# Performance work log

Hardware: AMD Instinct MI355X
Metric: run time of the kernel (lower is better)

The kernel has to match this reference:

```python
import jax, jax.numpy as jnp
import numpy as np

B, H, W, CIN, COUT, KH, KW = 16, 64, 64, 256, 256, 3, 3


def setup_inputs() -> dict:
    key = jax.random.key(0)
    k1, k2, k3 = jax.random.split(key, 3)
    x = jax.random.normal(k1, (B, H, W, CIN), dtype=jnp.float32)
    style = jax.random.normal(k2, (B, CIN), dtype=jnp.float32)
    # glorot-ish scale for the base kernel
    kernel = jax.random.normal(k3, (KH, KW, CIN, COUT), dtype=jnp.float32) * 0.05
    return {"x": x, "style": style, "kernel": kernel}


def reference(x, style, kernel):
    b = x.shape[0]
    cout = kernel.shape[-1]
    # Modulate: per-sample weights [B, kh, kw, Cin, Cout]
    w = kernel[None] * (style[:, None, None, :, None] + 1.0)
    # Demodulate: L2 normalize over (kh, kw, Cin) per (sample, out-channel)
    w = w / jnp.sqrt(jnp.sum(jnp.square(w), axis=(1, 2, 3), keepdims=True) + 1e-8)
    # Batch-as-groups grouped conv: x -> [1, B*Cin, H, W]
    xg = jnp.transpose(x, (0, 3, 1, 2)).reshape(1, -1, x.shape[1], x.shape[2])
    # w -> [kh, kw, Cin, B*Cout]
    wg = jnp.transpose(w, (1, 2, 3, 0, 4)).reshape(w.shape[1], w.shape[2], w.shape[3], -1)
    y = jax.lax.conv_general_dilated(
        xg, wg,
        window_strides=(1, 1),
        padding='SAME',
        dimension_numbers=('NCHW', 'HWIO', 'NCHW'),
        feature_group_count=b,
    )
    # [1, B*Cout, H, W] -> [B, H, W, Cout]
    y = y.reshape(b, cout, y.shape[2], y.shape[3])
    return jnp.transpose(y, (0, 2, 3, 1))
```

## Files before the change

### kernel.cpp

```cpp
#include <hip/hip_runtime.h>


#define HH 64
#define WW 64
#define CI 256
#define CO 256
#define XP 66
#define CIPITCH 40
#define XCOLS 66

typedef float    f32x4 __attribute__((ext_vector_type(4)));
typedef _Float16 f16x8 __attribute__((ext_vector_type(8)));
typedef __fp16   fp16x2 __attribute__((ext_vector_type(2)));

__device__ __forceinline__ unsigned pk2(float a, float b) {
    fp16x2 h = __builtin_amdgcn_cvt_pkrtz(a, b);
    return __builtin_bit_cast(unsigned, h);
}

__global__ __launch_bounds__(256) void prep(
    const float* __restrict__ kern,
    const float* __restrict__ style,
    ushort* __restrict__ Wt2,
    float* __restrict__ scale2)
{
    __shared__ ushort tile[64][65];
    __shared__ float  sqt[64][65];
    __shared__ float  st2l[16][64];

    const int kt = blockIdx.x >> 2;
    const int ct = blockIdx.x & 3;
    const int k0 = kt * 64, c0 = ct * 64;
    const int ci0 = k0 & 255;
    const int tid = threadIdx.x;
    const int r = tid >> 2, q = tid & 3;

    #pragma unroll
    for (int p = 0; p < 4; ++p) {
        const int i = p * 256 + tid;
        const int bb = i >> 6, rr = i & 63;
        const float s = style[bb * CI + ci0 + rr] + 1.0f;
        st2l[bb][rr] = s * s;
    }

    const float* src = kern + (size_t)(k0 + r) * CO + c0 + q * 16;
    #pragma unroll
    for (int j = 0; j < 16; ++j) {
        const float v = src[j];
        _Float16 h = (_Float16)v;
        tile[q * 16 + j][r] = __builtin_bit_cast(unsigned short, h);
        sqt[r][q * 16 + j] = v * v;
    }
    __syncthreads();

    const int co_w = c0 + r;
    #pragma unroll
    for (int j = 0; j < 16; ++j) {
        const int k   = k0 + q * 16 + j;
        const int t9  = k >> 8;
        const int rem = k & 255;
        const int cc  = rem >> 5;
        const int fq  = (rem >> 3) & 3;
        const int e   = k & 7;
        Wt2[((((size_t)cc * 9 + t9) * 4 + fq) * 256 + co_w) * 8 + e] =
            tile[r][q * 16 + j];
    }

    const int co = tid & 63;
    const int bq = tid >> 6;
    float acc[4] = {0.f, 0.f, 0.f, 0.f};
    #pragma unroll 4
    for (int rr = 0; rr < 64; ++rr) {
        const float s = sqt[rr][co];
        #pragma unroll
        for (int bb = 0; bb < 4; ++bb)
            acc[bb] += s * st2l[bq * 4 + bb][rr];
    }
    #pragma unroll
    for (int bb = 0; bb < 4; ++bb)
        atomicAdd(&scale2[(bq * 4 + bb) * CO + c0 + co], acc[bb]);
}

__global__ __launch_bounds__(256) void xmod_k(
    const float* __restrict__ x,
    const float* __restrict__ style,
    ushort* __restrict__ Xm)
{
    const int b  = blockIdx.x / XP;
    const int hh = blockIdx.x - b * XP;
    const int tid = threadIdx.x;
    ushort* dst = Xm + ((size_t)(b * XP + hh)) * XP * CI;

    if (hh == 0 || hh == XP - 1) {
        const uint4 z = {0, 0, 0, 0};
        #pragma unroll
        for (int p = 0; p < 9; ++p) {
            const int t = p * 256 + tid;
            if (t < 2112) *(uint4*)(dst + t * 8) = z;
        }
        return;
    }

    const int l = tid & 63;
    const int q = tid >> 6;
    const int ci0 = l * 4;
    const int rg = hh - 1;

    f32x4 st = *(const f32x4*)(style + b * CI + ci0);
    st.x += 1.f; st.y += 1.f; st.z += 1.f; st.w += 1.f;

    const float* srow = x + ((size_t)(b * HH + rg)) * WW * CI + ci0;
    #pragma unroll
    for (int k = 0; k < 17; ++k) {
        const int cc = q + 4 * k;
        if (cc < XP) {
            uint2 u = {0, 0};
            if (cc >= 1 && cc <= WW) {
                const f32x4 v = *(const f32x4*)(srow + (size_t)(cc - 1) * CI);
                const f32x4 m = v * st;
                u.x = pk2(m.x, m.y);
                u.y = pk2(m.z, m.w);
            }
            *(uint2*)(dst + cc * CI + ci0) = u;
        }
    }
}

__global__ __launch_bounds__(256, 3) void gemm_dma(
    const ushort* __restrict__ Xm,
    const ushort* __restrict__ Wt2,
    const float* __restrict__ scale2,
    float* __restrict__ y)
{
    __shared__ __align__(16) ushort xs[10240];
    __shared__ __align__(16) ushort bs[3 * 4096];

    const int tid  = threadIdx.x;
    const int lane = tid & 63;
    const int wave = tid >> 6;

    const int mtile = blockIdx.x >> 1;
    const int n0    = (blockIdx.x & 1) * 128;
    const int p0    = mtile * 128;
    const int b     = p0 >> 12;
    const int h0    = (p0 >> 6) & 63;

    const int wm = (wave & 1) * 64;
    const int wn = (wave >> 1) * 64;
    const int fr = lane & 15;
    const int fq = lane >> 4;

    const ushort* xb = Xm + (size_t)b * XP * XP * CI;

    auto issue_xs = [&](int cn) {
        #pragma unroll
        for (int p = 0; p < 5; ++p) {
            const int task = p * 256 + tid;
            const int rc = task >> 2;
            const int ch = (task & 3) ^ ((rc >> 1) & 3);
            const int off = (rc < 264)
                ? (((h0 + rc / 66) * XP + (rc % 66)) * CI + ch * 8 + cn * 32)
                : 0;
            const ushort* g = xb + off;
            const ushort* l = xs + (p * 256 + (tid & ~63)) * 8;
            __builtin_amdgcn_global_load_lds(
                (const __attribute__((address_space(1))) void*)g,
                (__attribute__((address_space(3))) void*)l,
                16, 0, 0);
        }
    };

    auto issue_tile = [&](int cn, int t9n, int bufn) {
        const ushort* gb = Wt2 + ((size_t)((cn * 9 + t9n) * 4) * 256 + n0) * 8;
        #pragma unroll
        for (int p = 0; p < 2; ++p) {
            const int task = p * 256 + tid;
            const ushort* g = gb + (size_t)(((task >> 7) << 8) + (task & 127)) * 8;
            const ushort* l = bs + bufn * 4096 + (p * 256 + (tid & ~63)) * 8;
            __builtin_amdgcn_global_load_lds(
                (const __attribute__((address_space(1))) void*)g,
                (__attribute__((address_space(3))) void*)l,
                16, 0, 0);
        }
    };

    f32x4 acc[4][4] = {};

    issue_xs(0);
    issue_tile(0, 0, 0);
    issue_tile(0, 1, 1);

    for (int c = 0; c < 8; ++c) {
        #pragma unroll
        for (int t9 = 0; t9 < 9; ++t9) {
            if (c == 7 && t9 == 8)
                asm volatile("s_waitcnt vmcnt(0) lgkmcnt(0)" ::: "memory");
            else
                asm volatile("s_waitcnt vmcnt(2) lgkmcnt(0)" ::: "memory");
            __builtin_amdgcn_s_barrier();

            const int dh  = t9 / 3;
            const int dw  = t9 - dh * 3;
            const int buf = t9 % 3;

            if (t9 < 8) {
                const int t2 = (t9 + 2 >= 9) ? t9 - 7 : t9 + 2;
                const int c2 = (t9 >= 7) ? c + 1 : c;
                if (c2 < 8) issue_tile(c2, t2, t2 % 3);

                f16x8 af[4], bf[4];
                #pragma unroll
                for (int i = 0; i < 4; ++i) {
                    const int mb = wm + i * 16;
                    const int rc = ((mb >> 6) + dh) * XCOLS + (mb & 63) + fr + dw;
                    af[i] = *(const f16x8*)(xs + rc * 32 + ((fq ^ ((rc >> 1) & 3)) * 8));
                }
                #pragma unroll
                for (int j = 0; j < 4; ++j)
                    bf[j] = *(const f16x8*)(bs + buf * 4096 + fq * 1024
                                            + (wn + j * 16 + fr) * 8);
                __builtin_amdgcn_s_setprio(1);
                #pragma unroll
                for (int i = 0; i < 4; ++i)
                    #pragma unroll
                    for (int j = 0; j < 4; ++j)
                        acc[i][j] = __builtin_amdgcn_mfma_f32_16x16x32_f16(
                            af[i], bf[j], acc[i][j], 0, 0, 0);
                __builtin_amdgcn_s_setprio(0);
            } else {
                f16x8 af[4], bf[4];
                #pragma unroll
                for (int i = 0; i < 4; ++i) {
                    const int mb = wm + i * 16;
                    const int rc = ((mb >> 6) + dh) * XCOLS + (mb & 63) + fr + dw;
                    af[i] = *(const f16x8*)(xs + rc * 32 + ((fq ^ ((rc >> 1) & 3)) * 8));
                }
                #pragma unroll
                for (int j = 0; j < 4; ++j)
                    bf[j] = *(const f16x8*)(bs + buf * 4096 + fq * 1024
                                            + (wn + j * 16 + fr) * 8);
                if (c < 7) {
                    asm volatile("s_waitcnt lgkmcnt(0)" ::: "memory");
                    __builtin_amdgcn_s_barrier();
                    issue_xs(c + 1);
                    issue_tile(c + 1, 1, 1);
                }
                __builtin_amdgcn_s_setprio(1);
                #pragma unroll
                for (int i = 0; i < 4; ++i)
                    #pragma unroll
                    for (int j = 0; j < 4; ++j)
                        acc[i][j] = __builtin_amdgcn_mfma_f32_16x16x32_f16(
                            af[i], bf[j], acc[i][j], 0, 0, 0);
                __builtin_amdgcn_s_setprio(0);
            }
        }
    }

    float sc[4];
    #pragma unroll
    for (int j = 0; j < 4; ++j)
        sc[j] = __frsqrt_rn(scale2[b * CO + n0 + wn + j * 16 + fr] + 1e-8f);
    #pragma unroll
    for (int i = 0; i < 4; ++i) {
        const int m_base = p0 + wm + i * 16 + fq * 4;
        #pragma unroll
        for (int j = 0; j < 4; ++j) {
            float* yp = y + (size_t)m_base * CO + n0 + wn + j * 16 + fr;
            #pragma unroll
            for (int r = 0; r < 4; ++r)
                yp[(size_t)r * CO] = acc[i][j][r] * sc[j];
        }
    }
}

__global__ __launch_bounds__(256) void gemm_lds(
    const float* __restrict__ x,
    const ushort* __restrict__ Wt2,
    const float* __restrict__ style,
    const float* __restrict__ scale2,
    float* __restrict__ y)
{
    __shared__ __align__(16) ushort xsf[4 * XCOLS * CIPITCH];
    __shared__ __align__(16) ushort bs[3 * 4096];
    __shared__ float s_style[CI];

    const int tid  = threadIdx.x;
    const int lane = tid & 63;
    const int wave = tid >> 6;

    const int mtile = blockIdx.x >> 1;
    const int n0    = (blockIdx.x & 1) * 128;
    const int p0    = mtile * 128;
    const int b     = p0 >> 12;
    const int h0    = (p0 >> 6) & 63;

    s_style[tid] = style[b * CI + tid] + 1.0f;

    const int wm = (wave & 1) * 64;
    const int wn = (wave >> 1) * 64;
    const int fr = lane & 15;
    const int fq = lane >> 4;
    const int xlane = fr * CIPITCH + fq * 8;

    auto issue_tile = [&](int cn, int t9n, int bufn) {
        const ushort* gb = Wt2 + ((size_t)((cn * 9 + t9n) * 4) * 256 + n0) * 8;
        #pragma unroll
        for (int p = 0; p < 2; ++p) {
            const int task = p * 256 + tid;
            const ushort* g = gb + (size_t)(((task >> 7) << 8) + (task & 127)) * 8;
            const ushort* l = bs + bufn * 4096 + (p * 256 + (tid & ~63)) * 8;
            __builtin_amdgcn_global_load_lds(
                (const __attribute__((address_space(1))) void*)g,
                (__attribute__((address_space(3))) void*)l,
                16, 0, 0);
        }
    };

    f32x4 acc[4][4] = {};

    issue_tile(0, 0, 0);
    issue_tile(0, 1, 1);

    for (int c = 0; c < 8; ++c) {
        #pragma unroll
        for (int t9 = 0; t9 < 9; ++t9) {
            asm volatile("s_waitcnt vmcnt(2) lgkmcnt(0)" ::: "memory");
            __builtin_amdgcn_s_barrier();

            if (t9 == 0) {
                #pragma unroll
                for (int p = 0; p < 9; ++p) {
                    const int task = p * 256 + tid;
                    if (task < 2112) {
                        const int rowcol = task >> 3;
                        const int chunk  = task & 7;
                        const int row = rowcol / XCOLS;
                        const int col = rowcol - row * XCOLS;
                        const int rg = h0 - 1 + row;
                        const int cg = col - 1;
                        f32x4 v = {0.f, 0.f, 0.f, 0.f};
                        if ((unsigned)rg < 64u && (unsigned)cg < 64u)
                            v = *(const f32x4*)(x + ((size_t)((b * HH + rg) * WW + cg)) * CI
                                                  + c * 32 + chunk * 4);
                        const f32x4 st = *(const f32x4*)(s_style + c * 32 + chunk * 4);
                        const f32x4 m = v * st;
                        uint2 u;
                        u.x = pk2(m.x, m.y);
                        u.y = pk2(m.z, m.w);
                        *(uint2*)(xsf + rowcol * CIPITCH + chunk * 4) = u;
                    }
                }
                asm volatile("s_waitcnt lgkmcnt(0)" ::: "memory");
                __builtin_amdgcn_s_barrier();
            }

            {
                const int t2 = (t9 + 2 >= 9) ? t9 - 7 : t9 + 2;
                const int c2 = (t9 >= 7) ? c + 1 : c;
                if (c2 < 8) issue_tile(c2, t2, t2 % 3);
            }

            const int buf = t9 % 3;
            const int dh  = t9 / 3;
            const int dw  = t9 - dh * 3;

            f16x8 af[4], bf[4];
            #pragma unroll
            for (int i = 0; i < 4; ++i) {
                const int mb   = wm + i * 16;
                const int mrow = (mb >> 6) + dh;
                const int mcol = (mb & 63) + dw;
                af[i] = *(const f16x8*)(xsf + (mrow * XCOLS + mcol) * CIPITCH + xlane);
            }
            #pragma unroll
            for (int j = 0; j < 4; ++j)
                bf[j] = *(const f16x8*)(bs + buf * 4096 + fq * 1024
                                        + (wn + j * 16 + fr) * 8);
            #pragma unroll
            for (int i = 0; i < 4; ++i)
                #pragma unroll
                for (int j = 0; j < 4; ++j)
                    acc[i][j] = __builtin_amdgcn_mfma_f32_16x16x32_f16(
                        af[i], bf[j], acc[i][j], 0, 0, 0);
        }
    }

    float sc[4];
    #pragma unroll
    for (int j = 0; j < 4; ++j)
        sc[j] = __frsqrt_rn(scale2[b * CO + n0 + wn + j * 16 + fr] + 1e-8f);
    #pragma unroll
    for (int i = 0; i < 4; ++i) {
        const int m_base = p0 + wm + i * 16 + fq * 4;
        #pragma unroll
        for (int j = 0; j < 4; ++j) {
            float* yp = y + (size_t)m_base * CO + n0 + wn + j * 16 + fr;
            #pragma unroll
            for (int r = 0; r < 4; ++r)
                yp[(size_t)r * CO] = acc[i][j][r] * sc[j];
        }
    }
}

extern "C" void kernel_launch(void* const* d_in, const int* in_sizes, int n_in,
                              void* d_out, int out_size, void* d_ws, size_t ws_size,
                              hipStream_t stream) {
    const float* x     = (const float*)d_in[0];
    const float* style = (const float*)d_in[1];
    const float* kern  = (const float*)d_in[2];
    float* out = (float*)d_out;

    float*  scale2 = (float*)d_ws;
    ushort* Wt2    = (ushort*)((char*)d_ws + 16384);

    const size_t xm_off  = 16384 + 1179648;
    const size_t xm_size = (size_t)16 * XP * XP * CI * 2;

    hipMemsetAsync(scale2, 0, 16 * CO * sizeof(float), stream);
    prep<<<144, 256, 0, stream>>>(kern, style, Wt2, scale2);

    if (ws_size >= xm_off + xm_size) {
        ushort* Xm = (ushort*)((char*)d_ws + xm_off);
        xmod_k<<<16 * XP, 256, 0, stream>>>(x, style, Xm);
        gemm_dma<<<512 * 2, 256, 0, stream>>>(Xm, Wt2, scale2, out);
    } else {
        gemm_lds<<<512 * 2, 256, 0, stream>>>(x, Wt2, style, scale2, out);
    }
}
```

Measured before the change: 209.0 us.

## Give each wave private double-buffered weight tiles to drop per-step block barriers

```diff
diff --git a/kernel.cpp b/kernel.cpp
--- a/kernel.cpp
+++ b/kernel.cpp
@@ -126,14 +126,14 @@
     }
 }
 
-__global__ __launch_bounds__(256, 3) void gemm_dma(
+__global__ __launch_bounds__(256) void gemm_dma(
     const ushort* __restrict__ Xm,
     const ushort* __restrict__ Wt2,
     const float* __restrict__ scale2,
     float* __restrict__ y)
 {
     __shared__ __align__(16) ushort xs[10240];
-    __shared__ __align__(16) ushort bs[3 * 4096];
+    __shared__ __align__(16) ushort bsw[4][2][2048];
 
     const int tid  = threadIdx.x;
     const int lane = tid & 63;
@@ -170,13 +170,13 @@
         }
     };
 
-    auto issue_tile = [&](int cn, int t9n, int bufn) {
-        const ushort* gb = Wt2 + ((size_t)((cn * 9 + t9n) * 4) * 256 + n0) * 8;
-        #pragma unroll
-        for (int p = 0; p < 2; ++p) {
-            const int task = p * 256 + tid;
-            const ushort* g = gb + (size_t)(((task >> 7) << 8) + (task & 127)) * 8;
-            const ushort* l = bs + bufn * 4096 + (p * 256 + (tid & ~63)) * 8;
+    auto issue_bs = [&](int T, int bufn) {
+        const ushort* gb = Wt2 + (size_t)T * 8192 + (size_t)(n0 + wn) * 8
+                           + (size_t)lane * 8;
+        #pragma unroll
+        for (int q = 0; q < 4; ++q) {
+            const ushort* g = gb + q * 2048;
+            const ushort* l = &bsw[wave][bufn][q * 512];
             __builtin_amdgcn_global_load_lds(
                 (const __attribute__((address_space(1))) void*)g,
                 (__attribute__((address_space(3))) void*)l,
@@ -187,72 +187,49 @@
     f32x4 acc[4][4] = {};
 
     issue_xs(0);
-    issue_tile(0, 0, 0);
-    issue_tile(0, 1, 1);
+    issue_bs(0, 0);
 
     for (int c = 0; c < 8; ++c) {
         #pragma unroll
         for (int t9 = 0; t9 < 9; ++t9) {
-            if (c == 7 && t9 == 8)
-                asm volatile("s_waitcnt vmcnt(0) lgkmcnt(0)" ::: "memory");
+            const int T = c * 9 + t9;
+
+            if (T < 71) issue_bs(T + 1, (T + 1) & 1);
+
+            if (t9 == 0)
+                asm volatile("s_waitcnt vmcnt(4)\n\ts_barrier" ::: "memory");
+            else if (T == 71)
+                asm volatile("s_waitcnt vmcnt(0)" ::: "memory");
             else
-                asm volatile("s_waitcnt vmcnt(2) lgkmcnt(0)" ::: "memory");
-            __builtin_amdgcn_s_barrier();
+                asm volatile("s_waitcnt vmcnt(4)" ::: "memory");
 
             const int dh  = t9 / 3;
             const int dw  = t9 - dh * 3;
-            const int buf = t9 % 3;
-
-            if (t9 < 8) {
-                const int t2 = (t9 + 2 >= 9) ? t9 - 7 : t9 + 2;
-                const int c2 = (t9 >= 7) ? c + 1 : c;
-                if (c2 < 8) issue_tile(c2, t2, t2 % 3);
-
-                f16x8 af[4], bf[4];
-                #pragma unroll
-                for (int i = 0; i < 4; ++i) {
-                    const int mb = wm + i * 16;
-                    const int rc = ((mb >> 6) + dh) * XCOLS + (mb & 63) + fr + dw;
-                    af[i] = *(const f16x8*)(xs + rc * 32 + ((fq ^ ((rc >> 1) & 3)) * 8));
-                }
+            const int buf = T & 1;
+
+            f16x8 af[4], bf[4];
+            #pragma unroll
+            for (int i = 0; i < 4; ++i) {
+                const int mb = wm + i * 16;
+                const int rc = ((mb >> 6) + dh) * XCOLS + (mb & 63) + fr + dw;
+                af[i] = *(const f16x8*)(xs + rc * 32 + ((fq ^ ((rc >> 1) & 3)) * 8));
+            }
+            #pragma unroll
+            for (int j = 0; j < 4; ++j)
+                bf[j] = *(const f16x8*)(&bsw[wave][buf][fq * 512 + (j * 16 + fr) * 8]);
+
+            __builtin_amdgcn_s_setprio(1);
+            #pragma unroll
+            for (int i = 0; i < 4; ++i)
                 #pragma unroll
                 for (int j = 0; j < 4; ++j)
-                    bf[j] = *(const f16x8*)(bs + buf * 4096 + fq * 1024
-                                            + (wn + j * 16 + fr) * 8);
-                __builtin_amdgcn_s_setprio(1);
-                #pragma unroll
-                for (int i = 0; i < 4; ++i)
-                    #pragma unroll
-                    for (int j = 0; j < 4; ++j)
-                        acc[i][j] = __builtin_amdgcn_mfma_f32_16x16x32_f16(
-                            af[i], bf[j], acc[i][j], 0, 0, 0);
-                __builtin_amdgcn_s_setprio(0);
-            } else {
-                f16x8 af[4], bf[4];
-                #pragma unroll
-                for (int i = 0; i < 4; ++i) {
-                    const int mb = wm + i * 16;
-                    const int rc = ((mb >> 6) + dh) * XCOLS + (mb & 63) + fr + dw;
-                    af[i] = *(const f16x8*)(xs + rc * 32 + ((fq ^ ((rc >> 1) & 3)) * 8));
-                }
-                #pragma unroll
-                for (int j = 0; j < 4; ++j)
-                    bf[j] = *(const f16x8*)(bs + buf * 4096 + fq * 1024
-                                            + (wn + j * 16 + fr) * 8);
-                if (c < 7) {
-                    asm volatile("s_waitcnt lgkmcnt(0)" ::: "memory");
-                    __builtin_amdgcn_s_barrier();
-                    issue_xs(c + 1);
-                    issue_tile(c + 1, 1, 1);
-                }
-                __builtin_amdgcn_s_setprio(1);
-                #pragma unroll
-                for (int i = 0; i < 4; ++i)
-                    #pragma unroll
-                    for (int j = 0; j < 4; ++j)
-                        acc[i][j] = __builtin_amdgcn_mfma_f32_16x16x32_f16(
-                            af[i], bf[j], acc[i][j], 0, 0, 0);
-                __builtin_amdgcn_s_setprio(0);
+                    acc[i][j] = __builtin_amdgcn_mfma_f32_16x16x32_f16(
+                        af[i], bf[j], acc[i][j], 0, 0, 0);
+            __builtin_amdgcn_s_setprio(0);
+
+            if (t9 == 8 && c < 7) {
+                asm volatile("s_waitcnt lgkmcnt(0)\n\ts_barrier" ::: "memory");
+                issue_xs(c + 1);
             }
         }
     }
```

Measured after the change: 216.6 us. 3.6% more time.
